# Kernel tuning notes

Hardware: AMD Instinct MI355X
Metric: run time of the kernel (lower is better)

## Reference

```python
import jax, jax.numpy as jnp
import numpy as np

NUM_CLASSES = 80


def _bce_logits(x, y):
    # numerically stable BCEWithLogits, elementwise
    return jnp.maximum(x, 0.0) - x * y + jnp.log1p(jnp.exp(-jnp.abs(x)))


def _iou_center(b1, b2):
    # boxes in (cx, cy, w, h) format, last dim = 4; returns IoU, last dim dropped
    b1x1 = b1[..., 0] - b1[..., 2] / 2
    b1y1 = b1[..., 1] - b1[..., 3] / 2
    b1x2 = b1[..., 0] + b1[..., 2] / 2
    b1y2 = b1[..., 1] + b1[..., 3] / 2
    b2x1 = b2[..., 0] - b2[..., 2] / 2
    b2y1 = b2[..., 1] - b2[..., 3] / 2
    b2x2 = b2[..., 0] + b2[..., 2] / 2
    b2y2 = b2[..., 1] + b2[..., 3] / 2
    iw = jnp.clip(jnp.minimum(b1x2, b2x2) - jnp.maximum(b1x1, b2x1), 0.0)
    ih = jnp.clip(jnp.minimum(b1y2, b2y2) - jnp.maximum(b1y1, b2y1), 0.0)
    inter = iw * ih
    union = (b1x2 - b1x1) * (b1y2 - b1y1) + (b2x2 - b2x1) * (b2y2 - b2y1) - inter
    return inter / (union + 1e-16)


def setup_inputs() -> dict:
    key = jax.random.key(0)
    kp, ko, kxy, kwh, kc, ka = jax.random.split(key, 6)
    B, A, S = 32, 3, 52
    predictions = jax.random.normal(kp, (B, A, S, S, 5 + NUM_CLASSES), dtype=jnp.float32)
    obj_flag = jax.random.bernoulli(ko, 0.3, (B, A, S, S, 1)).astype(jnp.float32)
    xy = jax.random.uniform(kxy, (B, A, S, S, 2), dtype=jnp.float32)
    wh = jax.random.uniform(kwh, (B, A, S, S, 2), minval=0.05, maxval=1.5, dtype=jnp.float32)
    cls = jax.random.randint(kc, (B, A, S, S, 1), 0, NUM_CLASSES).astype(jnp.float32)
    target = jnp.concatenate([obj_flag, xy, wh, cls], axis=-1)
    anchors = jax.random.uniform(ka, (3, 2), minval=0.1, maxval=1.0, dtype=jnp.float32)
    return {"predictions": predictions, "target": target, "anchors": anchors}


def reference(predictions, target, anchors):
    obj = (target[..., 0] == 1).astype(predictions.dtype)    # [B,3,S,S]
    noobj = (target[..., 0] == 0).astype(predictions.dtype)  # [B,3,S,S]
    n_obj = jnp.sum(obj)
    n_noobj = jnp.sum(noobj)

    anchors_r = anchors.reshape(1, 3, 1, 1, 2)
    pred_obj = predictions[..., 0]
    tgt_obj = target[..., 0]

    # noobj BCE (masked mean over noobj cells)
    no_detection = jnp.sum(_bce_logits(pred_obj, tgt_obj) * noobj) / n_noobj

    # decoded boxes and IoU (detached)
    pred_xy = jax.nn.sigmoid(predictions[..., 1:3])
    pred_wh_dec = jnp.exp(predictions[..., 3:5]) * anchors_r
    box_preds = jnp.concatenate([pred_xy, pred_wh_dec], axis=-1)
    ious = jax.lax.stop_gradient(_iou_center(box_preds, target[..., 1:5]))  # [B,3,S,S]

    # obj BCE against IoU-scaled targets (masked mean over obj cells)
    detection = jnp.sum(_bce_logits(pred_obj, ious * tgt_obj) * obj) / n_obj

    # box MSE: sigmoid(xy) & raw wh vs target xy & log(wh/anchors)
    pred_box = jnp.concatenate([pred_xy, predictions[..., 3:5]], axis=-1)
    tgt_box = jnp.concatenate(
        [target[..., 1:3], jnp.log(1e-16 + target[..., 3:5] / anchors_r)], axis=-1)
    box = jnp.sum(((pred_box - tgt_box) ** 2) * obj[..., None]) / (4.0 * n_obj)

    # classification CE (masked mean over obj cells)
    logp = jax.nn.log_softmax(predictions[..., 5:], axis=-1)
    labels = target[..., 5].astype(jnp.int32)
    nll = -jnp.take_along_axis(logp, labels[..., None], axis=-1)[..., 0]
    classification = jnp.sum(nll * obj) / n_obj

    return box + detection + no_detection + classification
```

## Files before the change

kernel.cpp:

```cpp
#include <hip/hip_runtime.h>

#define TILE      64
#define NTHREADS  256
#define STRIDE    85
#define NCLS      80
#define SSPAN     2704
#define NANCH     3
#define MAXGRID   2028

__device__ __forceinline__ float wave_reduce(float v) {
    #pragma unroll
    for (int off = 32; off > 0; off >>= 1)
        v += __shfl_down(v, off, 64);
    return v;
}

__global__ __launch_bounds__(NTHREADS) void loss_partial(
    const float* __restrict__ pred, const float* __restrict__ tgt,
    const float* __restrict__ anchors, float* __restrict__ partial,
    int n_cells, int n_tiles)
{
    __shared__ float lds_p[TILE * STRIDE];
    __shared__ float lds_t[TILE * 6];
    __shared__ float red[4][6];

    const int tid  = threadIdx.x;
    const int lane = tid & 63;
    const int wid  = tid >> 6;
    const int cell_l = tid >> 2;
    const int part   = tid & 3;

    float a_obj = 0.f, a_nobj = 0.f, a_bceo = 0.f, a_bceno = 0.f,
          a_box = 0.f, a_cls = 0.f;

    for (int tile = blockIdx.x; tile < n_tiles; tile += gridDim.x) {
        const int base = tile * TILE;

        if (base + TILE <= n_cells) {
            const float4* gp = (const float4*)(pred + (size_t)base * STRIDE);
            float4* lp = (float4*)lds_p;
            for (int i = tid; i < (TILE * STRIDE) / 4; i += NTHREADS) lp[i] = gp[i];
            const float4* gt = (const float4*)(tgt + (size_t)base * 6);
            float4* lt = (float4*)lds_t;
            if (tid < (TILE * 6) / 4) lt[tid] = gt[tid];
        } else {
            const int nv = n_cells - base;
            for (int i = tid; i < nv * STRIDE; i += NTHREADS)
                lds_p[i] = pred[(size_t)base * STRIDE + i];
            for (int i = tid; i < nv * 6; i += NTHREADS)
                lds_t[i] = tgt[(size_t)base * 6 + i];
        }
        __syncthreads();

        const int cell_g = base + cell_l;
        const bool active = (cell_g < n_cells);

        float v[20];
        const float* cp = lds_p + cell_l * STRIDE + 5 + part * 20;
        #pragma unroll
        for (int k = 0; k < 20; ++k) v[k] = cp[k];
        float mx = v[0];
        #pragma unroll
        for (int k = 1; k < 20; ++k) mx = fmaxf(mx, v[k]);
        mx = fmaxf(mx, __shfl_xor(mx, 1, 64));
        mx = fmaxf(mx, __shfl_xor(mx, 2, 64));
        float se = 0.f;
        #pragma unroll
        for (int k = 0; k < 20; ++k) se += __expf(v[k] - mx);
        se += __shfl_xor(se, 1, 64);
        se += __shfl_xor(se, 2, 64);

        if (part == 0 && active) {
            const float* pc = lds_p + cell_l * STRIDE;
            const float* tc = lds_t + cell_l * 6;
            const float p0 = pc[0], t0 = tc[0];
            const float bce_base = fmaxf(p0, 0.f) + log1pf(expf(-fabsf(p0)));
            if (t0 == 0.0f) { a_nobj += 1.f; a_bceno += bce_base; }
            if (t0 == 1.0f) {
                a_obj += 1.f;
                const int aidx = (cell_g / SSPAN) % NANCH;
                const float aw = anchors[aidx * 2], ah = anchors[aidx * 2 + 1];
                const float p1 = pc[1], p2 = pc[2], p3 = pc[3], p4 = pc[4];
                const float t1 = tc[1], t2 = tc[2], t3 = tc[3], t4 = tc[4];
                const float sx = 1.f / (1.f + expf(-p1));
                const float sy = 1.f / (1.f + expf(-p2));
                const float pw = expf(p3) * aw, ph = expf(p4) * ah;
                const float b1x1 = sx - pw * 0.5f, b1x2 = sx + pw * 0.5f;
                const float b1y1 = sy - ph * 0.5f, b1y2 = sy + ph * 0.5f;
                const float b2x1 = t1 - t3 * 0.5f, b2x2 = t1 + t3 * 0.5f;
                const float b2y1 = t2 - t4 * 0.5f, b2y2 = t2 + t4 * 0.5f;
                const float iw = fmaxf(fminf(b1x2, b2x2) - fmaxf(b1x1, b2x1), 0.f);
                const float ih = fmaxf(fminf(b1y2, b2y2) - fmaxf(b1y1, b2y1), 0.f);
                const float inter = iw * ih;
                const float uni = (b1x2 - b1x1) * (b1y2 - b1y1)
                                + (b2x2 - b2x1) * (b2y2 - b2y1) - inter;
                const float iou = inter / (uni + 1e-16f);
                a_bceo += bce_base - p0 * iou;
                const float lw = logf(1e-16f + t3 / aw);
                const float lh = logf(1e-16f + t4 / ah);
                const float d0 = sx - t1, d1 = sy - t2, d2 = p3 - lw, d3 = p4 - lh;
                a_box += d0 * d0 + d1 * d1 + d2 * d2 + d3 * d3;
                const int label = (int)tc[5];
                a_cls += (mx + logf(se)) - pc[5 + label];
            }
        }
        __syncthreads();
    }

    float vals[6] = {a_obj, a_nobj, a_bceo, a_bceno, a_box, a_cls};
    #pragma unroll
    for (int k = 0; k < 6; ++k) {
        const float r = wave_reduce(vals[k]);
        if (lane == 0) red[wid][k] = r;
    }
    __syncthreads();
    if (tid == 0) {
        #pragma unroll
        for (int k = 0; k < 6; ++k)
            partial[blockIdx.x * 6 + k] =
                red[0][k] + red[1][k] + red[2][k] + red[3][k];
    }
}

__global__ __launch_bounds__(NTHREADS) void loss_final(
    const float* __restrict__ partial, int nblocks, float* __restrict__ out)
{
    __shared__ float red[4][6];
    const int tid = threadIdx.x, lane = tid & 63, wid = tid >> 6;
    float s[6] = {0.f, 0.f, 0.f, 0.f, 0.f, 0.f};
    for (int i = tid; i < nblocks; i += NTHREADS) {
        #pragma unroll
        for (int k = 0; k < 6; ++k) s[k] += partial[i * 6 + k];
    }
    #pragma unroll
    for (int k = 0; k < 6; ++k) {
        const float r = wave_reduce(s[k]);
        if (lane == 0) red[wid][k] = r;
    }
    __syncthreads();
    if (tid == 0) {
        float t[6];
        #pragma unroll
        for (int k = 0; k < 6; ++k)
            t[k] = red[0][k] + red[1][k] + red[2][k] + red[3][k];
        const float n_obj = t[0], n_noobj = t[1];
        const float detection = t[2] / n_obj;
        const float no_det    = t[3] / n_noobj;
        const float box       = t[4] / (4.f * n_obj);
        const float cls       = t[5] / n_obj;
        out[0] = box + detection + no_det + cls;
    }
}

extern "C" void kernel_launch(void* const* d_in, const int* in_sizes, int n_in,
                              void* d_out, int out_size, void* d_ws, size_t ws_size,
                              hipStream_t stream) {
    const float* pred    = (const float*)d_in[0];
    const float* tgt     = (const float*)d_in[1];
    const float* anchors = (const float*)d_in[2];
    float* out = (float*)d_out;

    const int n_cells = in_sizes[1] / 6;
    const int n_tiles = (n_cells + TILE - 1) / TILE;
    const int grid = n_tiles < MAXGRID ? n_tiles : MAXGRID;
    float* partial = (float*)d_ws;

    loss_partial<<<grid, NTHREADS, 0, stream>>>(pred, tgt, anchors, partial,
                                                n_cells, n_tiles);
    loss_final<<<1, NTHREADS, 0, stream>>>(partial, grid, out);
}
```

Baseline: 148.3 us.

## Register-prefetch next tile while computing current tile, handle tail separately

Loads of the next tile are issued into registers before the current tile is computed, then written to LDS at the start of the next iteration. This overlaps global loads with compute in the grid-stride loop. Partial tiles are moved to a separate tail path in block 0 that reads straight from global memory, and anchors are preloaded into registers. Several expf/logf calls become fast intrinsics. The trade-off is higher register pressure from 7 float4 prefetch registers per thread, which could reduce occupancy, plus slightly lower accuracy from the intrinsics.

```diff
diff --git a/kernel.cpp b/kernel.cpp
--- a/kernel.cpp
+++ b/kernel.cpp
@@ -3,10 +3,10 @@
 #define TILE      64
 #define NTHREADS  256
 #define STRIDE    85
-#define NCLS      80
 #define SSPAN     2704
-#define NANCH     3
 #define MAXGRID   2028
+#define PF4       ((TILE*STRIDE)/4)
+#define TF4       ((TILE*6)/4)
 
 __device__ __forceinline__ float wave_reduce(float v) {
     #pragma unroll
@@ -18,45 +18,56 @@
 __global__ __launch_bounds__(NTHREADS) void loss_partial(
     const float* __restrict__ pred, const float* __restrict__ tgt,
     const float* __restrict__ anchors, float* __restrict__ partial,
-    int n_cells, int n_tiles)
+    int n_full, int n_rem)
 {
     __shared__ float lds_p[TILE * STRIDE];
     __shared__ float lds_t[TILE * 6];
     __shared__ float red[4][6];
 
-    const int tid  = threadIdx.x;
-    const int lane = tid & 63;
-    const int wid  = tid >> 6;
+    const int tid    = threadIdx.x;
+    const int lane   = tid & 63;
+    const int wid    = tid >> 6;
     const int cell_l = tid >> 2;
     const int part   = tid & 3;
 
+    const float aw0 = anchors[0], ah0 = anchors[1];
+    const float aw1 = anchors[2], ah1 = anchors[3];
+    const float aw2 = anchors[4], ah2 = anchors[5];
+
     float a_obj = 0.f, a_nobj = 0.f, a_bceo = 0.f, a_bceno = 0.f,
           a_box = 0.f, a_cls = 0.f;
 
-    for (int tile = blockIdx.x; tile < n_tiles; tile += gridDim.x) {
-        const int base = tile * TILE;
-
-        if (base + TILE <= n_cells) {
-            const float4* gp = (const float4*)(pred + (size_t)base * STRIDE);
-            float4* lp = (float4*)lds_p;
-            for (int i = tid; i < (TILE * STRIDE) / 4; i += NTHREADS) lp[i] = gp[i];
-            const float4* gt = (const float4*)(tgt + (size_t)base * 6);
-            float4* lt = (float4*)lds_t;
-            if (tid < (TILE * 6) / 4) lt[tid] = gt[tid];
-        } else {
-            const int nv = n_cells - base;
-            for (int i = tid; i < nv * STRIDE; i += NTHREADS)
-                lds_p[i] = pred[(size_t)base * STRIDE + i];
-            for (int i = tid; i < nv * 6; i += NTHREADS)
-                lds_t[i] = tgt[(size_t)base * 6 + i];
-        }
+    float4 rp[6];
+    float4 rt;
+
+    auto prefetch = [&](int t) {
+        const float4* gp = (const float4*)(pred + (size_t)t * (TILE * STRIDE));
+        #pragma unroll
+        for (int j = 0; j < 5; ++j) rp[j] = gp[tid + j * NTHREADS];
+        if (tid < PF4 - 5 * NTHREADS) rp[5] = gp[tid + 5 * NTHREADS];
+        const float4* gt = (const float4*)(tgt + (size_t)t * (TILE * 6));
+        if (tid < TF4) rt = gt[tid];
+    };
+    auto stow = [&]() {
+        float4* lp = (float4*)lds_p;
+        #pragma unroll
+        for (int j = 0; j < 5; ++j) lp[tid + j * NTHREADS] = rp[j];
+        if (tid < PF4 - 5 * NTHREADS) lp[tid + 5 * NTHREADS] = rp[5];
+        if (tid < TF4) ((float4*)lds_t)[tid] = rt;
+    };
+
+    int t = blockIdx.x;
+    if (t < n_full) prefetch(t);
+
+    for (; t < n_full; t += gridDim.x) {
         __syncthreads();
-
-        const int cell_g = base + cell_l;
-        const bool active = (cell_g < n_cells);
-
+        stow();
+        const int tn = t + gridDim.x;
+        if (tn < n_full) prefetch(tn);
+        __syncthreads();
+
+        const float* cp = lds_p + cell_l * STRIDE + 5 + part * 20;
         float v[20];
-        const float* cp = lds_p + cell_l * STRIDE + 5 + part * 20;
         #pragma unroll
         for (int k = 0; k < 20; ++k) v[k] = cp[k];
         float mx = v[0];
@@ -70,21 +81,23 @@
         se += __shfl_xor(se, 1, 64);
         se += __shfl_xor(se, 2, 64);
 
-        if (part == 0 && active) {
+        if (part == 0) {
             const float* pc = lds_p + cell_l * STRIDE;
             const float* tc = lds_t + cell_l * 6;
             const float p0 = pc[0], t0 = tc[0];
-            const float bce_base = fmaxf(p0, 0.f) + log1pf(expf(-fabsf(p0)));
+            const float bce_base = fmaxf(p0, 0.f) + log1pf(__expf(-fabsf(p0)));
             if (t0 == 0.0f) { a_nobj += 1.f; a_bceno += bce_base; }
             if (t0 == 1.0f) {
                 a_obj += 1.f;
-                const int aidx = (cell_g / SSPAN) % NANCH;
-                const float aw = anchors[aidx * 2], ah = anchors[aidx * 2 + 1];
+                const int cell_g = t * TILE + cell_l;
+                const int aidx = (cell_g / SSPAN) % 3;
+                const float aw = aidx == 0 ? aw0 : (aidx == 1 ? aw1 : aw2);
+                const float ah = aidx == 0 ? ah0 : (aidx == 1 ? ah1 : ah2);
                 const float p1 = pc[1], p2 = pc[2], p3 = pc[3], p4 = pc[4];
                 const float t1 = tc[1], t2 = tc[2], t3 = tc[3], t4 = tc[4];
-                const float sx = 1.f / (1.f + expf(-p1));
-                const float sy = 1.f / (1.f + expf(-p2));
-                const float pw = expf(p3) * aw, ph = expf(p4) * ah;
+                const float sx = 1.f / (1.f + __expf(-p1));
+                const float sy = 1.f / (1.f + __expf(-p2));
+                const float pw = __expf(p3) * aw, ph = __expf(p4) * ah;
                 const float b1x1 = sx - pw * 0.5f, b1x2 = sx + pw * 0.5f;
                 const float b1y1 = sy - ph * 0.5f, b1y2 = sy + ph * 0.5f;
                 const float b2x1 = t1 - t3 * 0.5f, b2x2 = t1 + t3 * 0.5f;
@@ -101,10 +114,62 @@
                 const float d0 = sx - t1, d1 = sy - t2, d2 = p3 - lw, d3 = p4 - lh;
                 a_box += d0 * d0 + d1 * d1 + d2 * d2 + d3 * d3;
                 const int label = (int)tc[5];
-                a_cls += (mx + logf(se)) - pc[5 + label];
+                a_cls += (mx + __logf(se)) - pc[5 + label];
             }
         }
-        __syncthreads();
+    }
+
+    if (blockIdx.x == 0 && n_rem > 0 && cell_l < n_rem) {
+        const int cell_g = n_full * TILE + cell_l;
+        const float* cp = pred + (size_t)cell_g * STRIDE + 5 + part * 20;
+        float v[20];
+        #pragma unroll
+        for (int k = 0; k < 20; ++k) v[k] = cp[k];
+        float mx = v[0];
+        #pragma unroll
+        for (int k = 1; k < 20; ++k) mx = fmaxf(mx, v[k]);
+        mx = fmaxf(mx, __shfl_xor(mx, 1, 64));
+        mx = fmaxf(mx, __shfl_xor(mx, 2, 64));
+        float se = 0.f;
+        #pragma unroll
+        for (int k = 0; k < 20; ++k) se += __expf(v[k] - mx);
+        se += __shfl_xor(se, 1, 64);
+        se += __shfl_xor(se, 2, 64);
+        if (part == 0) {
+            const float* pc = pred + (size_t)cell_g * STRIDE;
+            const float* tc = tgt + (size_t)cell_g * 6;
+            const float p0 = pc[0], t0 = tc[0];
+            const float bce_base = fmaxf(p0, 0.f) + log1pf(__expf(-fabsf(p0)));
+            if (t0 == 0.0f) { a_nobj += 1.f; a_bceno += bce_base; }
+            if (t0 == 1.0f) {
+                a_obj += 1.f;
+                const int aidx = (cell_g / SSPAN) % 3;
+                const float aw = aidx == 0 ? aw0 : (aidx == 1 ? aw1 : aw2);
+                const float ah = aidx == 0 ? ah0 : (aidx == 1 ? ah1 : ah2);
+                const float p1 = pc[1], p2 = pc[2], p3 = pc[3], p4 = pc[4];
+                const float t1 = tc[1], t2 = tc[2], t3 = tc[3], t4 = tc[4];
+                const float sx = 1.f / (1.f + __expf(-p1));
+                const float sy = 1.f / (1.f + __expf(-p2));
+                const float pw = __expf(p3) * aw, ph = __expf(p4) * ah;
+                const float b1x1 = sx - pw * 0.5f, b1x2 = sx + pw * 0.5f;
+                const float b1y1 = sy - ph * 0.5f, b1y2 = sy + ph * 0.5f;
+                const float b2x1 = t1 - t3 * 0.5f, b2x2 = t1 + t3 * 0.5f;
+                const float b2y1 = t2 - t4 * 0.5f, b2y2 = t2 + t4 * 0.5f;
+                const float iw = fmaxf(fminf(b1x2, b2x2) - fmaxf(b1x1, b2x1), 0.f);
+                const float ih = fmaxf(fminf(b1y2, b2y2) - fmaxf(b1y1, b2y1), 0.f);
+                const float inter = iw * ih;
+                const float uni = (b1x2 - b1x1) * (b1y2 - b1y1)
+                                + (b2x2 - b2x1) * (b2y2 - b2y1) - inter;
+                const float iou = inter / (uni + 1e-16f);
+                a_bceo += bce_base - p0 * iou;
+                const float lw = logf(1e-16f + t3 / aw);
+                const float lh = logf(1e-16f + t4 / ah);
+                const float d0 = sx - t1, d1 = sy - t2, d2 = p3 - lw, d3 = p4 - lh;
+                a_box += d0 * d0 + d1 * d1 + d2 * d2 + d3 * d3;
+                const int label = (int)tc[5];
+                a_cls += (mx + __logf(se)) - pc[5 + label];
+            }
+        }
     }
 
     float vals[6] = {a_obj, a_nobj, a_bceo, a_bceno, a_box, a_cls};
@@ -144,11 +209,8 @@
         for (int k = 0; k < 6; ++k)
             t[k] = red[0][k] + red[1][k] + red[2][k] + red[3][k];
         const float n_obj = t[0], n_noobj = t[1];
-        const float detection = t[2] / n_obj;
-        const float no_det    = t[3] / n_noobj;
-        const float box       = t[4] / (4.f * n_obj);
-        const float cls       = t[5] / n_obj;
-        out[0] = box + detection + no_det + cls;
+        out[0] = t[2] / n_obj + t[3] / n_noobj
+               + t[4] / (4.f * n_obj) + t[5] / n_obj;
     }
 }
 
@@ -161,11 +223,12 @@
     float* out = (float*)d_out;
 
     const int n_cells = in_sizes[1] / 6;
-    const int n_tiles = (n_cells + TILE - 1) / TILE;
-    const int grid = n_tiles < MAXGRID ? n_tiles : MAXGRID;
+    const int n_full  = n_cells / TILE;
+    const int n_rem   = n_cells % TILE;
+    const int grid = n_full < MAXGRID ? (n_full > 0 ? n_full : 1) : MAXGRID;
     float* partial = (float*)d_ws;
 
     loss_partial<<<grid, NTHREADS, 0, stream>>>(pred, tgt, anchors, partial,
-                                                n_cells, n_tiles);
+                                                n_full, n_rem);
     loss_final<<<1, NTHREADS, 0, stream>>>(partial, grid, out);
 }
```

Result: slower. 163.8 us (+10.4%).

## Skip loading class logits for non-object cells using wave-level ballot processing

Applied to the files above, without the earlier changes.

Replaces the LDS tile staging of all predictions with one wave per 64-cell group. Each lane reads only its objectness logit and target. A ballot over object cells then drives a wave-cooperative softmax and box computation per object cell, with the next cell's row prefetched. This avoids reading the class logits of non-object cells and removes block barriers. In exchange it makes strided scalar loads and serialises object cells within a wave.

```diff
diff --git a/kernel.cpp b/kernel.cpp
--- a/kernel.cpp
+++ b/kernel.cpp
@@ -1,12 +1,9 @@
 #include <hip/hip_runtime.h>
 
-#define TILE      64
 #define NTHREADS  256
 #define STRIDE    85
-#define NCLS      80
 #define SSPAN     2704
-#define NANCH     3
-#define MAXGRID   2028
+#define NEG_HUGE  -3.0e38f
 
 __device__ __forceinline__ float wave_reduce(float v) {
     #pragma unroll
@@ -18,93 +15,116 @@
 __global__ __launch_bounds__(NTHREADS) void loss_partial(
     const float* __restrict__ pred, const float* __restrict__ tgt,
     const float* __restrict__ anchors, float* __restrict__ partial,
-    int n_cells, int n_tiles)
+    int n_cells, int ngroups)
 {
-    __shared__ float lds_p[TILE * STRIDE];
-    __shared__ float lds_t[TILE * 6];
     __shared__ float red[4][6];
 
     const int tid  = threadIdx.x;
     const int lane = tid & 63;
     const int wid  = tid >> 6;
-    const int cell_l = tid >> 2;
-    const int part   = tid & 3;
+
+    const float aw0 = anchors[0], ah0 = anchors[1];
+    const float aw1 = anchors[2], ah1 = anchors[3];
+    const float aw2 = anchors[4], ah2 = anchors[5];
 
     float a_obj = 0.f, a_nobj = 0.f, a_bceo = 0.f, a_bceno = 0.f,
           a_box = 0.f, a_cls = 0.f;
 
-    for (int tile = blockIdx.x; tile < n_tiles; tile += gridDim.x) {
-        const int base = tile * TILE;
+    const int gstride = gridDim.x * 4;
+    for (int g = blockIdx.x * 4 + wid; g < ngroups; g += gstride) {
+        const int cbase = g * 64;
+        const int cell  = cbase + lane;
+        const bool valid = cell < n_cells;
 
-        if (base + TILE <= n_cells) {
-            const float4* gp = (const float4*)(pred + (size_t)base * STRIDE);
-            float4* lp = (float4*)lds_p;
-            for (int i = tid; i < (TILE * STRIDE) / 4; i += NTHREADS) lp[i] = gp[i];
-            const float4* gt = (const float4*)(tgt + (size_t)base * 6);
-            float4* lt = (float4*)lds_t;
-            if (tid < (TILE * 6) / 4) lt[tid] = gt[tid];
-        } else {
-            const int nv = n_cells - base;
-            for (int i = tid; i < nv * STRIDE; i += NTHREADS)
-                lds_p[i] = pred[(size_t)base * STRIDE + i];
-            for (int i = tid; i < nv * 6; i += NTHREADS)
-                lds_t[i] = tgt[(size_t)base * 6 + i];
+        float t0 = -1.f, t1 = 0.f, t2 = 0.f, t3 = 0.f, t4 = 0.f, t5 = 0.f;
+        float p0 = 0.f;
+        if (valid) {
+            const float* tc = tgt + (size_t)cell * 6;
+            t0 = tc[0]; t1 = tc[1]; t2 = tc[2];
+            t3 = tc[3]; t4 = tc[4]; t5 = tc[5];
+            p0 = pred[(size_t)cell * STRIDE];
         }
-        __syncthreads();
+        const float bce_base = fmaxf(p0, 0.f) + log1pf(__expf(-fabsf(p0)));
+        if (t0 == 0.0f) { a_nobj += 1.f; a_bceno += bce_base; }
+        if (t0 == 1.0f) { a_obj  += 1.f; }
 
-        const int cell_g = base + cell_l;
-        const bool active = (cell_g < n_cells);
+        unsigned long long m = __ballot(t0 == 1.0f);
 
-        float v[20];
-        const float* cp = lds_p + cell_l * STRIDE + 5 + part * 20;
-        #pragma unroll
-        for (int k = 0; k < 20; ++k) v[k] = cp[k];
-        float mx = v[0];
-        #pragma unroll
-        for (int k = 1; k < 20; ++k) mx = fmaxf(mx, v[k]);
-        mx = fmaxf(mx, __shfl_xor(mx, 1, 64));
-        mx = fmaxf(mx, __shfl_xor(mx, 2, 64));
-        float se = 0.f;
-        #pragma unroll
-        for (int k = 0; k < 20; ++k) se += __expf(v[k] - mx);
-        se += __shfl_xor(se, 1, 64);
-        se += __shfl_xor(se, 2, 64);
+        int c0 = -1; float f1a = 0.f, f2a = 0.f;
+        if (m) {
+            c0 = __ffsll(m) - 1; m &= m - 1;
+            const float* b = pred + (size_t)(cbase + c0) * STRIDE;
+            f1a = b[1 + lane];
+            if (lane < 20) f2a = b[65 + lane];
+        }
+        while (c0 >= 0) {
+            int c1 = -1; float f1b = 0.f, f2b = 0.f;
+            if (m) {
+                c1 = __ffsll(m) - 1; m &= m - 1;
+                const float* b = pred + (size_t)(cbase + c1) * STRIDE;
+                f1b = b[1 + lane];
+                if (lane < 20) f2b = b[65 + lane];
+            }
+            {
+                const int cg = cbase + c0;
+                const float m1 = (lane >= 4) ? f1a : NEG_HUGE;
+                const float m2 = (lane < 20) ? f2a : NEG_HUGE;
+                float mx = fmaxf(m1, m2);
+                #pragma unroll
+                for (int o = 32; o; o >>= 1) mx = fmaxf(mx, __shfl_xor(mx, o, 64));
+                float e = ((lane >= 4) ? __expf(f1a - mx) : 0.f)
+                        + ((lane < 20) ? __expf(f2a - mx) : 0.f);
+                #pragma unroll
+                for (int o = 32; o; o >>= 1) e += __shfl_xor(e, o, 64);
 
-        if (part == 0 && active) {
-            const float* pc = lds_p + cell_l * STRIDE;
-            const float* tc = lds_t + cell_l * 6;
-            const float p0 = pc[0], t0 = tc[0];
-            const float bce_base = fmaxf(p0, 0.f) + log1pf(expf(-fabsf(p0)));
-            if (t0 == 0.0f) { a_nobj += 1.f; a_bceno += bce_base; }
-            if (t0 == 1.0f) {
-                a_obj += 1.f;
-                const int aidx = (cell_g / SSPAN) % NANCH;
-                const float aw = anchors[aidx * 2], ah = anchors[aidx * 2 + 1];
-                const float p1 = pc[1], p2 = pc[2], p3 = pc[3], p4 = pc[4];
-                const float t1 = tc[1], t2 = tc[2], t3 = tc[3], t4 = tc[4];
-                const float sx = 1.f / (1.f + expf(-p1));
-                const float sy = 1.f / (1.f + expf(-p2));
-                const float pw = expf(p3) * aw, ph = expf(p4) * ah;
+                const float tb1 = __shfl(t1, c0, 64), tb2 = __shfl(t2, c0, 64);
+                const float tb3 = __shfl(t3, c0, 64), tb4 = __shfl(t4, c0, 64);
+                const float tb5 = __shfl(t5, c0, 64);
+                const float pb0 = __shfl(p0, c0, 64);
+                const float bb  = __shfl(bce_base, c0, 64);
+                const float pp1 = __shfl(f1a, 0, 64), pp2 = __shfl(f1a, 1, 64);
+                const float pp3 = __shfl(f1a, 2, 64), pp4 = __shfl(f1a, 3, 64);
+
+                const int   label = (int)tb5;
+                const int   idx   = 5 + label;
+                const float s1 = __shfl(f1a, (idx - 1) & 63, 64);
+                const float s2 = __shfl(f2a, (idx - 65) & 63, 64);
+                const float lv = (idx <= 64) ? s1 : s2;
+
+                const int aidx = (cg / SSPAN) % 3;
+                const float aw = aidx == 0 ? aw0 : (aidx == 1 ? aw1 : aw2);
+                const float ah = aidx == 0 ? ah0 : (aidx == 1 ? ah1 : ah2);
+
+                const float sx = 1.f / (1.f + __expf(-pp1));
+                const float sy = 1.f / (1.f + __expf(-pp2));
+                const float pw = __expf(pp3) * aw, ph = __expf(pp4) * ah;
                 const float b1x1 = sx - pw * 0.5f, b1x2 = sx + pw * 0.5f;
                 const float b1y1 = sy - ph * 0.5f, b1y2 = sy + ph * 0.5f;
-                const float b2x1 = t1 - t3 * 0.5f, b2x2 = t1 + t3 * 0.5f;
-                const float b2y1 = t2 - t4 * 0.5f, b2y2 = t2 + t4 * 0.5f;
+                const float b2x1 = tb1 - tb3 * 0.5f, b2x2 = tb1 + tb3 * 0.5f;
+                const float b2y1 = tb2 - tb4 * 0.5f, b2y2 = tb2 + tb4 * 0.5f;
                 const float iw = fmaxf(fminf(b1x2, b2x2) - fmaxf(b1x1, b2x1), 0.f);
                 const float ih = fmaxf(fminf(b1y2, b2y2) - fmaxf(b1y1, b2y1), 0.f);
                 const float inter = iw * ih;
                 const float uni = (b1x2 - b1x1) * (b1y2 - b1y1)
                                 + (b2x2 - b2x1) * (b2y2 - b2y1) - inter;
                 const float iou = inter / (uni + 1e-16f);
-                a_bceo += bce_base - p0 * iou;
-                const float lw = logf(1e-16f + t3 / aw);
-                const float lh = logf(1e-16f + t4 / ah);
-                const float d0 = sx - t1, d1 = sy - t2, d2 = p3 - lw, d3 = p4 - lh;
-                a_box += d0 * d0 + d1 * d1 + d2 * d2 + d3 * d3;
-                const int label = (int)tc[5];
-                a_cls += (mx + logf(se)) - pc[5 + label];
+
+                const float vbceo = bb - pb0 * iou;
+                const float lw = logf(1e-16f + tb3 / aw);
+                const float lh = logf(1e-16f + tb4 / ah);
+                const float d0 = sx - tb1, d1 = sy - tb2;
+                const float d2 = pp3 - lw, d3 = pp4 - lh;
+                const float vbox = d0 * d0 + d1 * d1 + d2 * d2 + d3 * d3;
+                const float vcls = (mx + __logf(e)) - lv;
+
+                if (lane == c0) {
+                    a_bceo += vbceo;
+                    a_box  += vbox;
+                    a_cls  += vcls;
+                }
             }
+            c0 = c1; f1a = f1b; f2a = f2b;
         }
-        __syncthreads();
     }
 
     float vals[6] = {a_obj, a_nobj, a_bceo, a_bceno, a_box, a_cls};
@@ -144,11 +164,8 @@
         for (int k = 0; k < 6; ++k)
             t[k] = red[0][k] + red[1][k] + red[2][k] + red[3][k];
         const float n_obj = t[0], n_noobj = t[1];
-        const float detection = t[2] / n_obj;
-        const float no_det    = t[3] / n_noobj;
-        const float box       = t[4] / (4.f * n_obj);
-        const float cls       = t[5] / n_obj;
-        out[0] = box + detection + no_det + cls;
+        out[0] = t[2] / n_obj + t[3] / n_noobj
+               + t[4] / (4.f * n_obj) + t[5] / n_obj;
     }
 }
 
@@ -161,11 +178,13 @@
     float* out = (float*)d_out;
 
     const int n_cells = in_sizes[1] / 6;
-    const int n_tiles = (n_cells + TILE - 1) / TILE;
-    const int grid = n_tiles < MAXGRID ? n_tiles : MAXGRID;
+    const int ngroups = (n_cells + 63) / 64;
+    int grid = (ngroups + 3) / 4;
+    if (grid > 2048) grid = 2048;
+    if (grid < 1)    grid = 1;
     float* partial = (float*)d_ws;
 
     loss_partial<<<grid, NTHREADS, 0, stream>>>(pred, tgt, anchors, partial,
-                                                n_cells, n_tiles);
+                                                n_cells, ngroups);
     loss_final<<<1, NTHREADS, 0, stream>>>(partial, grid, out);
 }
```

Result: slower. 163.9 us (+10.5%).
